# Performance work log

Measured on AMD Instinct MI355X. Metric: run time of the kernel, lower is better.

Reference implementation:

```python
import jax, jax.numpy as jnp
import numpy as np

R, N, B = 3, 8192, 4096
IN_DIM, HID, OUT = 256, 128, 64
EPS = 1e-5


def _bn(x, g, b):
    # BatchNorm1d in training mode: biased batch stats over dim 0
    m = jnp.mean(x, axis=0)
    v = jnp.var(x, axis=0)
    return (x - m) * jax.lax.rsqrt(v + EPS) * g + b


def setup_inputs() -> dict:
    key = jax.random.key(0)
    k1, k2, k3, k4, k5 = jax.random.split(key, 5)
    features = jax.random.normal(k1, (N, IN_DIM), dtype=jnp.float32)
    u = jax.random.uniform(k2, (R, N, N), dtype=jnp.float32)
    adj = (u < 0.01).astype(jnp.float32)
    batch_nodes = jax.random.randint(k3, (B,), 0, N, dtype=jnp.int32)
    w1 = jax.random.uniform(k4, (IN_DIM, HID), dtype=jnp.float32)  # torch.rand init
    w2 = jax.random.uniform(k5, (HID, OUT), dtype=jnp.float32)
    return {
        "features": features, "adj": adj, "batch_nodes": batch_nodes,
        "w1": w1, "w2": w2,
        "gamma1": jnp.ones((IN_DIM,), jnp.float32), "beta1": jnp.zeros((IN_DIM,), jnp.float32),
        "gamma2": jnp.ones((OUT,), jnp.float32), "beta2": jnp.zeros((OUT,), jnp.float32),
    }


def reference(features, adj, batch_nodes, w1, w2, gamma1, beta1, gamma2, beta2):
    # gather batch subgraph
    x = features[batch_nodes]                       # [B, IN_DIM]
    bA = jnp.take(jnp.take(adj, batch_nodes, axis=1), batch_nodes, axis=2)  # [R, B, B]
    xn = _bn(x, gamma1, beta1)                      # shared across relations

    def per_relation(badj):
        A = badj + jnp.eye(B, dtype=badj.dtype)
        # D_mx.inverse().sqrt() of a diagonal degree matrix == diag(deg^-1/2)
        dinv = jax.lax.rsqrt(jnp.sum(A, axis=1))    # [B]
        A_hat = A * dinv[:, None] * dinv[None, :]   # D^-1/2 A D^-1/2
        h1 = jax.nn.sigmoid(jax.nn.elu((A_hat @ xn) @ w1))   # conv1 + sigmoid
        h2 = jax.nn.elu((A_hat @ h1) @ w2)                   # conv2
        return _bn(h2, gamma2, beta2)

    embed = jax.vmap(per_relation)(bA)              # [R, B, OUT]
    return jax.nn.relu(jnp.mean(embed, axis=0))     # [B, OUT]
```

## Files before the change

kernel.cpp:

```cpp
#include <hip/hip_runtime.h>
#include <hip/hip_bf16.h>

#define RR 3
#define NN 8192
#define BB 4096
#define IN_DIM 256
#define HID 128
#define OUT 64
#define CAPD 128
#define EPS 1e-5f
#define MWN (NN / 64)

__global__ __launch_bounds__(1024) void prep_k(const int* __restrict__ bn,
                                               unsigned long long* __restrict__ memb,
                                               unsigned short* __restrict__ rankg,
                                               unsigned short* __restrict__ nodeof,
                                               float* __restrict__ multf,
                                               int* __restrict__ Ucnt,
                                               unsigned short* __restrict__ pos2slot) {
    __shared__ int smult[NN];
    __shared__ unsigned short srank[NN];
    __shared__ unsigned long long smemb[MWN];
    __shared__ int sbase[MWN + 1];
    int t = threadIdx.x;
    for (int u = t; u < NN; u += 1024) smult[u] = 0;
    __syncthreads();
    for (int i = t; i < BB; i += 1024) atomicAdd(&smult[bn[i]], 1);
    __syncthreads();
    if (t < MWN) {
        unsigned long long w = 0;
        for (int b = 0; b < 64; ++b) if (smult[t * 64 + b]) w |= (1ull << b);
        smemb[t] = w;
        memb[t] = w;
    }
    __syncthreads();
    if (t == 0) {
        int acc = 0;
        for (int m = 0; m < MWN; ++m) { sbase[m] = acc; acc += (int)__popcll(smemb[m]); }
        sbase[MWN] = acc;
        *Ucnt = acc;
    }
    __syncthreads();
    if (t < MWN) {
        unsigned long long w = smemb[t];
        int p = sbase[t];
        while (w) {
            int b = __builtin_ctzll(w); w &= w - 1;
            int u = t * 64 + b;
            srank[u] = (unsigned short)p;
            rankg[u] = (unsigned short)p;
            nodeof[p] = (unsigned short)u;
            multf[p]  = (float)smult[u];
            ++p;
        }
    }
    __syncthreads();
    for (int i = t; i < BB; i += 1024) pos2slot[i] = srank[bn[i]];
}

__global__ __launch_bounds__(256) void bn1_stats_k(const float* __restrict__ feat,
                                                   const int* __restrict__ bn,
                                                   float* __restrict__ m1,
                                                   float* __restrict__ rs1) {
    int c = blockIdx.x;
    float s = 0.f, q = 0.f;
    for (int i = threadIdx.x; i < BB; i += 256) {
        float v = feat[(size_t)bn[i] * IN_DIM + c];
        s += v; q += v * v;
    }
    int lane = threadIdx.x & 63, wv = threadIdx.x >> 6;
    for (int o = 32; o; o >>= 1) { s += __shfl_down(s, o); q += __shfl_down(q, o); }
    __shared__ float ps[4], pq[4];
    if (lane == 0) { ps[wv] = s; pq[wv] = q; }
    __syncthreads();
    if (threadIdx.x == 0) {
        float S = ps[0] + ps[1] + ps[2] + ps[3];
        float Q = pq[0] + pq[1] + pq[2] + pq[3];
        float m = S / BB;
        float v = Q / BB - m * m;
        m1[c] = m;
        rs1[c] = rsqrtf(v + EPS);
    }
}

__global__ __launch_bounds__(256) void xn_c_k(const float* __restrict__ feat,
                                              const unsigned short* __restrict__ nodeof,
                                              const int* __restrict__ Ucnt,
                                              const float* __restrict__ m1,
                                              const float* __restrict__ rs1,
                                              const float* __restrict__ g1,
                                              const float* __restrict__ b1,
                                              float* __restrict__ xn_c) {
    int s = blockIdx.x;
    if (s >= *Ucnt) return;
    int u = nodeof[s];
    int c = threadIdx.x;
    float v = feat[(size_t)u * IN_DIM + c];
    xn_c[(size_t)s * IN_DIM + c] = (v - m1[c]) * rs1[c] * g1[c] + b1[c];
}

__global__ __launch_bounds__(256) void build_k(const float* __restrict__ adj,
                                               const unsigned short* __restrict__ nodeof,
                                               const int* __restrict__ Ucnt,
                                               const unsigned long long* __restrict__ memb,
                                               const unsigned short* __restrict__ rankg,
                                               const float* __restrict__ multf,
                                               unsigned short* __restrict__ cols,
                                               int* __restrict__ cnt,
                                               float* __restrict__ dinv) {
    int blk = blockIdx.x;
    int r = blk >> 12, s = blk & (BB - 1);
    if (s >= *Ucnt) return;
    int u = nodeof[s];
    __shared__ unsigned char nib[2048];
    __shared__ unsigned int rawb[256];
    __shared__ unsigned long long sel[MWN];
    __shared__ int sbase[MWN + 1];
    __shared__ float pdeg[4];
    int t = threadIdx.x;
    const float4* ar4 = (const float4*)(adj + ((size_t)r * NN + u) * NN);
    #pragma unroll
    for (int ch = 0; ch < 8; ++ch) {
        float4 v = ar4[ch * 256 + t];
        nib[ch * 256 + t] = (unsigned char)((v.x != 0.f) | ((v.y != 0.f) << 1) |
                                            ((v.z != 0.f) << 2) | ((v.w != 0.f) << 3));
    }
    __syncthreads();
    {
        unsigned long long x = *(const unsigned long long*)&nib[t * 8];
        x = (x | (x >> 4))  & 0x00FF00FF00FF00FFull;
        x = (x | (x >> 8))  & 0x0000FFFF0000FFFFull;
        x = (x | (x >> 16));
        rawb[t] = (unsigned int)x;
    }
    __syncthreads();
    if (t < MWN) {
        unsigned long long w = ((unsigned long long)rawb[2 * t + 1] << 32) | rawb[2 * t];
        sel[t] = w & memb[t];
    }
    __syncthreads();
    if (t < 64) {
        int p0 = (int)__popcll(sel[2 * t]);
        int p1 = (int)__popcll(sel[2 * t + 1]);
        int x = p0 + p1, xs = x;
        for (int o = 1; o < 64; o <<= 1) { int y = __shfl_up(xs, o); if (t >= o) xs += y; }
        sbase[2 * t]     = xs - x;
        sbase[2 * t + 1] = xs - p1;
        if (t == 63) sbase[MWN] = xs;
    }
    __syncthreads();
    float wdeg = 0.f;
    if (t < MWN) {
        unsigned long long w = sel[t];
        int p = sbase[t];
        unsigned short* cb = cols + (size_t)blk * CAPD;
        while (w) {
            int b = __builtin_ctzll(w); w &= w - 1;
            int v = t * 64 + b;
            int rv = rankg[v];
            if (p < CAPD) cb[p] = (unsigned short)rv;
            wdeg += multf[rv];
            ++p;
        }
    }
    int lane = t & 63, wv = t >> 6;
    for (int o = 32; o; o >>= 1) wdeg += __shfl_down(wdeg, o);
    if (lane == 0) pdeg[wv] = wdeg;
    __syncthreads();
    if (t == 0) {
        int tot = sbase[MWN];
        cnt[blk] = tot < CAPD ? tot : CAPD;
        dinv[blk] = rsqrtf(pdeg[0] + pdeg[1] + pdeg[2] + pdeg[3] + 1.0f);
    }
}

__global__ __launch_bounds__(256) void layer1_k(const float* __restrict__ xn_c,
                                                const unsigned short* __restrict__ cols,
                                                const int* __restrict__ cnt,
                                                const float* __restrict__ dinv,
                                                const float* __restrict__ multf,
                                                const int* __restrict__ Ucnt,
                                                const float* __restrict__ w1,
                                                float* __restrict__ h1) {
    int blk = blockIdx.x;
    int r = blk >> 12, s = blk & (BB - 1);
    if (s >= *Ucnt) return;
    int c = threadIdx.x;
    __shared__ unsigned short scl[CAPD];
    __shared__ float swl[CAPD];
    int n = cnt[blk];
    if (c < n) {
        int sl = cols[(size_t)blk * CAPD + c];
        scl[c] = (unsigned short)sl;
        swl[c] = multf[sl] * dinv[(r << 12) + sl];
    }
    __syncthreads();
    float di = dinv[blk];
    float acc = di * xn_c[(size_t)s * IN_DIM + c];
    #pragma unroll 4
    for (int k = 0; k < n; ++k) {
        acc += swl[k] * xn_c[(size_t)scl[k] * IN_DIM + c];
    }
    acc *= di;
    __shared__ float ys[IN_DIM];
    ys[c] = acc;
    __syncthreads();
    if (c < HID) {
        float z = 0.f;
        #pragma unroll 8
        for (int k = 0; k < IN_DIM; ++k) z += ys[k] * w1[k * HID + c];
        float e = z > 0.f ? z : expm1f(z);
        float h = 1.0f / (1.0f + expf(-e));
        h1[(size_t)blk * HID + c] = h;
    }
}

__global__ __launch_bounds__(128) void layer2_k(const float* __restrict__ h1,
                                                const unsigned short* __restrict__ cols,
                                                const int* __restrict__ cnt,
                                                const float* __restrict__ dinv,
                                                const float* __restrict__ multf,
                                                const int* __restrict__ Ucnt,
                                                const float* __restrict__ w2,
                                                float* __restrict__ h2) {
    int blk = blockIdx.x;
    int r = blk >> 12, s = blk & (BB - 1);
    if (s >= *Ucnt) return;
    int c = threadIdx.x;
    __shared__ unsigned short scl[CAPD];
    __shared__ float swl[CAPD];
    int n = cnt[blk];
    if (c < n) {
        int sl = cols[(size_t)blk * CAPD + c];
        scl[c] = (unsigned short)sl;
        swl[c] = multf[sl] * dinv[(r << 12) + sl];
    }
    __syncthreads();
    const float* h1r = h1 + ((size_t)r << 12) * HID;
    float di = dinv[blk];
    float acc = di * h1r[(size_t)s * HID + c];
    #pragma unroll 4
    for (int k = 0; k < n; ++k) {
        acc += swl[k] * h1r[(size_t)scl[k] * HID + c];
    }
    acc *= di;
    __shared__ float ys[HID];
    ys[c] = acc;
    __syncthreads();
    if (c < OUT) {
        float z = 0.f;
        #pragma unroll 8
        for (int k = 0; k < HID; ++k) z += ys[k] * w2[k * OUT + c];
        float e = z > 0.f ? z : expm1f(z);
        h2[(size_t)blk * OUT + c] = e;
    }
}

__global__ __launch_bounds__(256) void bn2_stats_k(const float* __restrict__ h2,
                                                   const float* __restrict__ multf,
                                                   const int* __restrict__ Ucnt,
                                                   float* __restrict__ m2,
                                                   float* __restrict__ rs2) {
    int ro = blockIdx.x;
    int r = ro >> 6, o = ro & (OUT - 1);
    int U = *Ucnt;
    float s = 0.f, q = 0.f;
    for (int sl = threadIdx.x; sl < U; sl += 256) {
        float m = multf[sl];
        float v = h2[(size_t)((r << 12) + sl) * OUT + o];
        s += m * v; q += m * v * v;
    }
    int lane = threadIdx.x & 63, wv = threadIdx.x >> 6;
    for (int off = 32; off; off >>= 1) { s += __shfl_down(s, off); q += __shfl_down(q, off); }
    __shared__ float ps[4], pq[4];
    if (lane == 0) { ps[wv] = s; pq[wv] = q; }
    __syncthreads();
    if (threadIdx.x == 0) {
        float S = ps[0] + ps[1] + ps[2] + ps[3];
        float Q = pq[0] + pq[1] + pq[2] + pq[3];
        float m = S / BB;
        float v = Q / BB - m * m;
        m2[ro] = m;
        rs2[ro] = rsqrtf(v + EPS);
    }
}

__global__ __launch_bounds__(256) void finalize_k(const float* __restrict__ h2,
                                                  const unsigned short* __restrict__ pos2slot,
                                                  const float* __restrict__ m2,
                                                  const float* __restrict__ rs2,
                                                  const float* __restrict__ g2,
                                                  const float* __restrict__ b2,
                                                  float* __restrict__ out) {
    int idx = blockIdx.x * 256 + threadIdx.x;
    if (idx >= BB * OUT) return;
    int i = idx >> 6, o = idx & (OUT - 1);
    int sl = pos2slot[i];
    float s = 0.f;
    for (int r = 0; r < RR; ++r) {
        float v = h2[(size_t)((r << 12) + sl) * OUT + o];
        s += (v - m2[r * OUT + o]) * rs2[r * OUT + o] * g2[o] + b2[o];
    }
    s *= (1.0f / RR);
    out[idx] = s > 0.f ? s : 0.f;
}

extern "C" void kernel_launch(void* const* d_in, const int* in_sizes, int n_in,
                              void* d_out, int out_size, void* d_ws, size_t ws_size,
                              hipStream_t stream) {
    const float* feat = (const float*)d_in[0];
    const float* adj  = (const float*)d_in[1];
    const int*   bn   = (const int*)d_in[2];
    const float* w1   = (const float*)d_in[3];
    const float* w2   = (const float*)d_in[4];
    const float* g1   = (const float*)d_in[5];
    const float* b1   = (const float*)d_in[6];
    const float* g2   = (const float*)d_in[7];
    const float* b2   = (const float*)d_in[8];
    float* out = (float*)d_out;

    char* ws = (char*)d_ws;
    size_t off = 0;
    auto alloc = [&](size_t bytes) { size_t o = off; off += (bytes + 255) & ~(size_t)255; return o; };
    unsigned long long* memb = (unsigned long long*)(ws + alloc(MWN * 8));
    unsigned short* rankg    = (unsigned short*)(ws + alloc(NN * 2));
    unsigned short* nodeof   = (unsigned short*)(ws + alloc(BB * 2));
    float* multf             = (float*)(ws + alloc(BB * 4));
    int* Ucnt                = (int*)(ws + alloc(4));
    unsigned short* pos2slot = (unsigned short*)(ws + alloc(BB * 2));
    float* m1                = (float*)(ws + alloc(IN_DIM * 4));
    float* rs1               = (float*)(ws + alloc(IN_DIM * 4));
    float* m2                = (float*)(ws + alloc(RR * OUT * 4));
    float* rs2               = (float*)(ws + alloc(RR * OUT * 4));
    float* xn_c              = (float*)(ws + alloc((size_t)BB * IN_DIM * 4));
    unsigned short* cols     = (unsigned short*)(ws + alloc((size_t)RR * BB * CAPD * 2));
    int* cnt                 = (int*)(ws + alloc((size_t)RR * BB * 4));
    float* dinv              = (float*)(ws + alloc((size_t)RR * BB * 4));
    float* h1                = (float*)(ws + alloc((size_t)RR * BB * HID * 4));
    float* h2                = (float*)(ws + alloc((size_t)RR * BB * OUT * 4));

    prep_k<<<1, 1024, 0, stream>>>(bn, memb, rankg, nodeof, multf, Ucnt, pos2slot);
    bn1_stats_k<<<IN_DIM, 256, 0, stream>>>(feat, bn, m1, rs1);
    xn_c_k<<<BB, 256, 0, stream>>>(feat, nodeof, Ucnt, m1, rs1, g1, b1, xn_c);
    build_k<<<RR * BB, 256, 0, stream>>>(adj, nodeof, Ucnt, memb, rankg, multf, cols, cnt, dinv);
    layer1_k<<<RR * BB, 256, 0, stream>>>(xn_c, cols, cnt, dinv, multf, Ucnt, w1, h1);
    layer2_k<<<RR * BB, 128, 0, stream>>>(h1, cols, cnt, dinv, multf, Ucnt, w2, h2);
    bn2_stats_k<<<RR * OUT, 256, 0, stream>>>(h2, multf, Ucnt, m2, rs2);
    finalize_k<<<(BB * OUT + 255) / 256, 256, 0, stream>>>(h2, pos2slot, m2, rs2, g2, b2, out);
}
```

Baseline: 176.5 us.

## Process four nodes per block in GCN layers and split BN1 stats reduction

layer1 and layer2 now handle four compacted nodes per block, one wavefront per node, using float4/float2 vectorized neighbor gathers. Each W1/W2 weight load is shared across two or four node rows, and block count and launch overhead drop. BN1 statistics are now computed over unique nodes weighted by multiplicity, using a two-stage partial and final reduction instead of one block per column with strided gathers. This adds an extra kernel launch and leaves a longer serial loop per wavefront when a node has high degree.

```diff
diff --git a/kernel.cpp b/kernel.cpp
--- a/kernel.cpp
+++ b/kernel.cpp
@@ -58,29 +58,38 @@
     for (int i = t; i < BB; i += 1024) pos2slot[i] = srank[bn[i]];
 }
 
-__global__ __launch_bounds__(256) void bn1_stats_k(const float* __restrict__ feat,
-                                                   const int* __restrict__ bn,
+__global__ __launch_bounds__(256) void bn1_partial_k(const float* __restrict__ feat,
+                                                     const unsigned short* __restrict__ nodeof,
+                                                     const float* __restrict__ multf,
+                                                     const int* __restrict__ Ucnt,
+                                                     float* __restrict__ partial) {
+    int b = blockIdx.x;
+    int c = threadIdx.x;
+    int U = *Ucnt;
+    float s = 0.f, q = 0.f;
+    for (int t = 0; t < 64; ++t) {
+        int sl = b * 64 + t;
+        if (sl >= U) break;
+        float m = multf[sl];
+        float v = feat[(size_t)nodeof[sl] * IN_DIM + c];
+        s += m * v; q += m * v * v;
+    }
+    partial[(size_t)(2 * b) * IN_DIM + c]     = s;
+    partial[(size_t)(2 * b + 1) * IN_DIM + c] = q;
+}
+
+__global__ __launch_bounds__(256) void bn1_final_k(const float* __restrict__ partial,
                                                    float* __restrict__ m1,
                                                    float* __restrict__ rs1) {
-    int c = blockIdx.x;
-    float s = 0.f, q = 0.f;
-    for (int i = threadIdx.x; i < BB; i += 256) {
-        float v = feat[(size_t)bn[i] * IN_DIM + c];
-        s += v; q += v * v;
-    }
-    int lane = threadIdx.x & 63, wv = threadIdx.x >> 6;
-    for (int o = 32; o; o >>= 1) { s += __shfl_down(s, o); q += __shfl_down(q, o); }
-    __shared__ float ps[4], pq[4];
-    if (lane == 0) { ps[wv] = s; pq[wv] = q; }
-    __syncthreads();
-    if (threadIdx.x == 0) {
-        float S = ps[0] + ps[1] + ps[2] + ps[3];
-        float Q = pq[0] + pq[1] + pq[2] + pq[3];
-        float m = S / BB;
-        float v = Q / BB - m * m;
-        m1[c] = m;
-        rs1[c] = rsqrtf(v + EPS);
-    }
+    int c = threadIdx.x;
+    float S = 0.f, Q = 0.f;
+    for (int b = 0; b < 64; ++b) {
+        S += partial[(size_t)(2 * b) * IN_DIM + c];
+        Q += partial[(size_t)(2 * b + 1) * IN_DIM + c];
+    }
+    float m = S / BB;
+    m1[c] = m;
+    rs1[c] = rsqrtf(Q / BB - m * m + EPS);
 }
 
 __global__ __launch_bounds__(256) void xn_c_k(const float* __restrict__ feat,
@@ -183,39 +192,55 @@
                                                 const float* __restrict__ w1,
                                                 float* __restrict__ h1) {
     int blk = blockIdx.x;
-    int r = blk >> 12, s = blk & (BB - 1);
-    if (s >= *Ucnt) return;
-    int c = threadIdx.x;
-    __shared__ unsigned short scl[CAPD];
-    __shared__ float swl[CAPD];
-    int n = cnt[blk];
-    if (c < n) {
-        int sl = cols[(size_t)blk * CAPD + c];
-        scl[c] = (unsigned short)sl;
-        swl[c] = multf[sl] * dinv[(r << 12) + sl];
-    }
-    __syncthreads();
-    float di = dinv[blk];
-    float acc = di * xn_c[(size_t)s * IN_DIM + c];
-    #pragma unroll 4
-    for (int k = 0; k < n; ++k) {
-        acc += swl[k] * xn_c[(size_t)scl[k] * IN_DIM + c];
-    }
-    acc *= di;
-    __shared__ float ys[IN_DIM];
-    ys[c] = acc;
-    __syncthreads();
-    if (c < HID) {
-        float z = 0.f;
-        #pragma unroll 8
-        for (int k = 0; k < IN_DIM; ++k) z += ys[k] * w1[k * HID + c];
-        float e = z > 0.f ? z : expm1f(z);
-        float h = 1.0f / (1.0f + expf(-e));
-        h1[(size_t)blk * HID + c] = h;
-    }
-}
-
-__global__ __launch_bounds__(128) void layer2_k(const float* __restrict__ h1,
+    int r = blk >> 10, base = (blk & 1023) << 2;
+    int U = *Ucnt;
+    int tid = threadIdx.x, lane = tid & 63, wv = tid >> 6;
+    __shared__ unsigned short scl[4][CAPD];
+    __shared__ float swl[4][CAPD];
+    __shared__ float ys[4][IN_DIM];
+    __shared__ float sdi[4];
+    int slot = base + wv;
+    int n = (slot < U) ? cnt[(r << 12) + slot] : 0;
+    if (lane == 0) sdi[wv] = (slot < U) ? dinv[(r << 12) + slot] : 0.f;
+    size_t cb = ((size_t)(r << 12) + slot) * CAPD;
+    for (int idx = lane; idx < n; idx += 64) {
+        int sl = cols[cb + idx];
+        scl[wv][idx] = (unsigned short)sl;
+        swl[wv][idx] = multf[sl] * dinv[(r << 12) + sl];
+    }
+    __syncthreads();
+    {
+        float di = sdi[wv];
+        float4 acc = make_float4(0.f, 0.f, 0.f, 0.f);
+        if (slot < U) {
+            float4 xv = ((const float4*)(xn_c + (size_t)slot * IN_DIM))[lane];
+            acc.x = di * xv.x; acc.y = di * xv.y; acc.z = di * xv.z; acc.w = di * xv.w;
+        }
+        #pragma unroll 4
+        for (int k = 0; k < n; ++k) {
+            float4 xv = ((const float4*)(xn_c + (size_t)scl[wv][k] * IN_DIM))[lane];
+            float wk = swl[wv][k];
+            acc.x += wk * xv.x; acc.y += wk * xv.y; acc.z += wk * xv.z; acc.w += wk * xv.w;
+        }
+        acc.x *= di; acc.y *= di; acc.z *= di; acc.w *= di;
+        *(float4*)&ys[wv][lane * 4] = acc;
+    }
+    __syncthreads();
+    int c = tid & 127, h = tid >> 7;
+    float z0 = 0.f, z1 = 0.f;
+    #pragma unroll 8
+    for (int k = 0; k < IN_DIM; ++k) {
+        float wvl = w1[k * HID + c];
+        z0 += ys[h][k] * wvl;
+        z1 += ys[h + 2][k] * wvl;
+    }
+    float e0 = z0 > 0.f ? z0 : expm1f(z0);
+    h1[((size_t)(r << 12) + base + h) * HID + c] = 1.f / (1.f + expf(-e0));
+    float e1 = z1 > 0.f ? z1 : expm1f(z1);
+    h1[((size_t)(r << 12) + base + h + 2) * HID + c] = 1.f / (1.f + expf(-e1));
+}
+
+__global__ __launch_bounds__(256) void layer2_k(const float* __restrict__ h1,
                                                 const unsigned short* __restrict__ cols,
                                                 const int* __restrict__ cnt,
                                                 const float* __restrict__ dinv,
@@ -224,36 +249,47 @@
                                                 const float* __restrict__ w2,
                                                 float* __restrict__ h2) {
     int blk = blockIdx.x;
-    int r = blk >> 12, s = blk & (BB - 1);
-    if (s >= *Ucnt) return;
-    int c = threadIdx.x;
-    __shared__ unsigned short scl[CAPD];
-    __shared__ float swl[CAPD];
-    int n = cnt[blk];
-    if (c < n) {
-        int sl = cols[(size_t)blk * CAPD + c];
-        scl[c] = (unsigned short)sl;
-        swl[c] = multf[sl] * dinv[(r << 12) + sl];
-    }
-    __syncthreads();
-    const float* h1r = h1 + ((size_t)r << 12) * HID;
-    float di = dinv[blk];
-    float acc = di * h1r[(size_t)s * HID + c];
-    #pragma unroll 4
-    for (int k = 0; k < n; ++k) {
-        acc += swl[k] * h1r[(size_t)scl[k] * HID + c];
-    }
-    acc *= di;
-    __shared__ float ys[HID];
-    ys[c] = acc;
-    __syncthreads();
-    if (c < OUT) {
-        float z = 0.f;
-        #pragma unroll 8
-        for (int k = 0; k < HID; ++k) z += ys[k] * w2[k * OUT + c];
-        float e = z > 0.f ? z : expm1f(z);
-        h2[(size_t)blk * OUT + c] = e;
-    }
+    int r = blk >> 10, base = (blk & 1023) << 2;
+    int U = *Ucnt;
+    int tid = threadIdx.x, lane = tid & 63, wv = tid >> 6;
+    __shared__ unsigned short scl[4][CAPD];
+    __shared__ float swl[4][CAPD];
+    __shared__ float ys[4][HID];
+    __shared__ float sdi[4];
+    int slot = base + wv;
+    int n = (slot < U) ? cnt[(r << 12) + slot] : 0;
+    if (lane == 0) sdi[wv] = (slot < U) ? dinv[(r << 12) + slot] : 0.f;
+    size_t cb = ((size_t)(r << 12) + slot) * CAPD;
+    for (int idx = lane; idx < n; idx += 64) {
+        int sl = cols[cb + idx];
+        scl[wv][idx] = (unsigned short)sl;
+        swl[wv][idx] = multf[sl] * dinv[(r << 12) + sl];
+    }
+    __syncthreads();
+    const float* h1r = h1 + ((size_t)(r << 12)) * HID;
+    {
+        float di = sdi[wv];
+        float2 acc = make_float2(0.f, 0.f);
+        if (slot < U) {
+            float2 xv = ((const float2*)(h1r + (size_t)slot * HID))[lane];
+            acc.x = di * xv.x; acc.y = di * xv.y;
+        }
+        #pragma unroll 4
+        for (int k = 0; k < n; ++k) {
+            float2 xv = ((const float2*)(h1r + (size_t)scl[wv][k] * HID))[lane];
+            float wk = swl[wv][k];
+            acc.x += wk * xv.x; acc.y += wk * xv.y;
+        }
+        acc.x *= di; acc.y *= di;
+        ys[wv][lane * 2] = acc.x; ys[wv][lane * 2 + 1] = acc.y;
+    }
+    __syncthreads();
+    int c = tid & 63, g = tid >> 6;
+    float z = 0.f;
+    #pragma unroll 8
+    for (int k = 0; k < HID; ++k) z += ys[g][k] * w2[k * OUT + c];
+    float e = z > 0.f ? z : expm1f(z);
+    h2[((size_t)(r << 12) + base + g) * OUT + c] = e;
 }
 
 __global__ __launch_bounds__(256) void bn2_stats_k(const float* __restrict__ h2,
@@ -328,6 +364,7 @@
     float* multf             = (float*)(ws + alloc(BB * 4));
     int* Ucnt                = (int*)(ws + alloc(4));
     unsigned short* pos2slot = (unsigned short*)(ws + alloc(BB * 2));
+    float* partial           = (float*)(ws + alloc(128 * IN_DIM * 4));
     float* m1                = (float*)(ws + alloc(IN_DIM * 4));
     float* rs1               = (float*)(ws + alloc(IN_DIM * 4));
     float* m2                = (float*)(ws + alloc(RR * OUT * 4));
@@ -340,11 +377,12 @@
     float* h2                = (float*)(ws + alloc((size_t)RR * BB * OUT * 4));
 
     prep_k<<<1, 1024, 0, stream>>>(bn, memb, rankg, nodeof, multf, Ucnt, pos2slot);
-    bn1_stats_k<<<IN_DIM, 256, 0, stream>>>(feat, bn, m1, rs1);
+    bn1_partial_k<<<64, 256, 0, stream>>>(feat, nodeof, multf, Ucnt, partial);
+    bn1_final_k<<<1, 256, 0, stream>>>(partial, m1, rs1);
     xn_c_k<<<BB, 256, 0, stream>>>(feat, nodeof, Ucnt, m1, rs1, g1, b1, xn_c);
     build_k<<<RR * BB, 256, 0, stream>>>(adj, nodeof, Ucnt, memb, rankg, multf, cols, cnt, dinv);
-    layer1_k<<<RR * BB, 256, 0, stream>>>(xn_c, cols, cnt, dinv, multf, Ucnt, w1, h1);
-    layer2_k<<<RR * BB, 128, 0, stream>>>(h1, cols, cnt, dinv, multf, Ucnt, w2, h2);
+    layer1_k<<<RR * (BB / 4), 256, 0, stream>>>(xn_c, cols, cnt, dinv, multf, Ucnt, w1, h1);
+    layer2_k<<<RR * (BB / 4), 256, 0, stream>>>(h1, cols, cnt, dinv, multf, Ucnt, w2, h2);
     bn2_stats_k<<<RR * OUT, 256, 0, stream>>>(h2, multf, Ucnt, m2, rs2);
     finalize_k<<<(BB * OUT + 255) / 256, 256, 0, stream>>>(h2, pos2slot, m2, rs2, g2, b2, out);
 }
```

New measurement: 198.5 us. 12.5% more time.

## Split aggregation and dense projection into separate kernels with batched row tiles

Applied to the files above, without the earlier changes.

The fused per-row layer kernels, which ran the sparse aggregation and the weight matvec in the same block, are split in two. The aggregation kernels now write the aggregated features to new intermediate buffers. New MLP kernels then multiply tiles of 16 rows by w1 and w2, so each weight load is reused across 8 or 4 rows per thread. Previously each row re-read the whole weight matrix with only half or a quarter of its threads active. The cost is two extra launches and extra global traffic to write and re-read the intermediates.

```diff
diff --git a/kernel.cpp b/kernel.cpp
--- a/kernel.cpp
+++ b/kernel.cpp
@@ -10,6 +10,7 @@
 #define CAPD 128
 #define EPS 1e-5f
 #define MWN (NN / 64)
+#define MLPB 16
 
 __global__ __launch_bounds__(1024) void prep_k(const int* __restrict__ bn,
                                                unsigned long long* __restrict__ memb,
@@ -174,14 +175,13 @@
     }
 }
 
-__global__ __launch_bounds__(256) void layer1_k(const float* __restrict__ xn_c,
-                                                const unsigned short* __restrict__ cols,
-                                                const int* __restrict__ cnt,
-                                                const float* __restrict__ dinv,
-                                                const float* __restrict__ multf,
-                                                const int* __restrict__ Ucnt,
-                                                const float* __restrict__ w1,
-                                                float* __restrict__ h1) {
+__global__ __launch_bounds__(256) void layer1_agg_k(const float* __restrict__ xn_c,
+                                                    const unsigned short* __restrict__ cols,
+                                                    const int* __restrict__ cnt,
+                                                    const float* __restrict__ dinv,
+                                                    const float* __restrict__ multf,
+                                                    const int* __restrict__ Ucnt,
+                                                    float* __restrict__ y1) {
     int blk = blockIdx.x;
     int r = blk >> 12, s = blk & (BB - 1);
     if (s >= *Ucnt) return;
@@ -201,28 +201,50 @@
     for (int k = 0; k < n; ++k) {
         acc += swl[k] * xn_c[(size_t)scl[k] * IN_DIM + c];
     }
-    acc *= di;
-    __shared__ float ys[IN_DIM];
-    ys[c] = acc;
-    __syncthreads();
-    if (c < HID) {
-        float z = 0.f;
-        #pragma unroll 8
-        for (int k = 0; k < IN_DIM; ++k) z += ys[k] * w1[k * HID + c];
-        float e = z > 0.f ? z : expm1f(z);
-        float h = 1.0f / (1.0f + expf(-e));
-        h1[(size_t)blk * HID + c] = h;
-    }
-}
-
-__global__ __launch_bounds__(128) void layer2_k(const float* __restrict__ h1,
-                                                const unsigned short* __restrict__ cols,
-                                                const int* __restrict__ cnt,
-                                                const float* __restrict__ dinv,
-                                                const float* __restrict__ multf,
-                                                const int* __restrict__ Ucnt,
-                                                const float* __restrict__ w2,
-                                                float* __restrict__ h2) {
+    y1[(size_t)blk * IN_DIM + c] = acc * di;
+}
+
+__global__ __launch_bounds__(256) void mlp1_k(const float* __restrict__ y1,
+                                              const int* __restrict__ Ucnt,
+                                              const float* __restrict__ w1,
+                                              float* __restrict__ h1) {
+    int blk = blockIdx.x;
+    int r = blk / (BB / MLPB), base = (blk % (BB / MLPB)) * MLPB;
+    int U = *Ucnt;
+    if (base >= U) return;
+    int t = threadIdx.x;
+    __shared__ float ys[MLPB][IN_DIM];
+    #pragma unroll
+    for (int s = 0; s < MLPB; ++s) {
+        int slot = base + s;
+        ys[s][t] = (slot < U) ? y1[((size_t)(r << 12) + slot) * IN_DIM + t] : 0.f;
+    }
+    __syncthreads();
+    int c = t & 127, g = t >> 7;
+    float acc[8] = {0.f};
+    for (int k = 0; k < IN_DIM; ++k) {
+        float wv = w1[k * HID + c];
+        #pragma unroll
+        for (int j = 0; j < 8; ++j) acc[j] += ys[g * 8 + j][k] * wv;
+    }
+    #pragma unroll
+    for (int j = 0; j < 8; ++j) {
+        int slot = base + g * 8 + j;
+        if (slot < U) {
+            float z = acc[j];
+            float e = z > 0.f ? z : expm1f(z);
+            h1[((size_t)(r << 12) + slot) * HID + c] = 1.f / (1.f + expf(-e));
+        }
+    }
+}
+
+__global__ __launch_bounds__(128) void layer2_agg_k(const float* __restrict__ h1,
+                                                    const unsigned short* __restrict__ cols,
+                                                    const int* __restrict__ cnt,
+                                                    const float* __restrict__ dinv,
+                                                    const float* __restrict__ multf,
+                                                    const int* __restrict__ Ucnt,
+                                                    float* __restrict__ y2) {
     int blk = blockIdx.x;
     int r = blk >> 12, s = blk & (BB - 1);
     if (s >= *Ucnt) return;
@@ -236,23 +258,46 @@
         swl[c] = multf[sl] * dinv[(r << 12) + sl];
     }
     __syncthreads();
-    const float* h1r = h1 + ((size_t)r << 12) * HID;
+    const float* h1r = h1 + ((size_t)(r << 12)) * HID;
     float di = dinv[blk];
     float acc = di * h1r[(size_t)s * HID + c];
     #pragma unroll 4
     for (int k = 0; k < n; ++k) {
         acc += swl[k] * h1r[(size_t)scl[k] * HID + c];
     }
-    acc *= di;
-    __shared__ float ys[HID];
-    ys[c] = acc;
-    __syncthreads();
-    if (c < OUT) {
-        float z = 0.f;
-        #pragma unroll 8
-        for (int k = 0; k < HID; ++k) z += ys[k] * w2[k * OUT + c];
-        float e = z > 0.f ? z : expm1f(z);
-        h2[(size_t)blk * OUT + c] = e;
+    y2[(size_t)blk * HID + c] = acc * di;
+}
+
+__global__ __launch_bounds__(256) void mlp2_k(const float* __restrict__ y2,
+                                              const int* __restrict__ Ucnt,
+                                              const float* __restrict__ w2,
+                                              float* __restrict__ h2) {
+    int blk = blockIdx.x;
+    int r = blk / (BB / MLPB), base = (blk % (BB / MLPB)) * MLPB;
+    int U = *Ucnt;
+    if (base >= U) return;
+    int t = threadIdx.x;
+    __shared__ float ys[MLPB][HID];
+    #pragma unroll
+    for (int s = t >> 7; s < MLPB; s += 2) {
+        int slot = base + s;
+        ys[s][t & 127] = (slot < U) ? y2[((size_t)(r << 12) + slot) * HID + (t & 127)] : 0.f;
+    }
+    __syncthreads();
+    int c = t & 63, g = t >> 6;
+    float acc[4] = {0.f};
+    for (int k = 0; k < HID; ++k) {
+        float wv = w2[k * OUT + c];
+        #pragma unroll
+        for (int j = 0; j < 4; ++j) acc[j] += ys[g * 4 + j][k] * wv;
+    }
+    #pragma unroll
+    for (int j = 0; j < 4; ++j) {
+        int slot = base + g * 4 + j;
+        if (slot < U) {
+            float z = acc[j];
+            h2[((size_t)(r << 12) + slot) * OUT + c] = z > 0.f ? z : expm1f(z);
+        }
     }
 }
 
@@ -336,15 +381,19 @@
     unsigned short* cols     = (unsigned short*)(ws + alloc((size_t)RR * BB * CAPD * 2));
     int* cnt                 = (int*)(ws + alloc((size_t)RR * BB * 4));
     float* dinv              = (float*)(ws + alloc((size_t)RR * BB * 4));
+    float* y1                = (float*)(ws + alloc((size_t)RR * BB * IN_DIM * 4));
     float* h1                = (float*)(ws + alloc((size_t)RR * BB * HID * 4));
+    float* y2                = (float*)(ws + alloc((size_t)RR * BB * HID * 4));
     float* h2                = (float*)(ws + alloc((size_t)RR * BB * OUT * 4));
 
     prep_k<<<1, 1024, 0, stream>>>(bn, memb, rankg, nodeof, multf, Ucnt, pos2slot);
     bn1_stats_k<<<IN_DIM, 256, 0, stream>>>(feat, bn, m1, rs1);
     xn_c_k<<<BB, 256, 0, stream>>>(feat, nodeof, Ucnt, m1, rs1, g1, b1, xn_c);
     build_k<<<RR * BB, 256, 0, stream>>>(adj, nodeof, Ucnt, memb, rankg, multf, cols, cnt, dinv);
-    layer1_k<<<RR * BB, 256, 0, stream>>>(xn_c, cols, cnt, dinv, multf, Ucnt, w1, h1);
-    layer2_k<<<RR * BB, 128, 0, stream>>>(h1, cols, cnt, dinv, multf, Ucnt, w2, h2);
+    layer1_agg_k<<<RR * BB, 256, 0, stream>>>(xn_c, cols, cnt, dinv, multf, Ucnt, y1);
+    mlp1_k<<<RR * (BB / MLPB), 256, 0, stream>>>(y1, Ucnt, w1, h1);
+    layer2_agg_k<<<RR * BB, 128, 0, stream>>>(h1, cols, cnt, dinv, multf, Ucnt, y2);
+    mlp2_k<<<RR * (BB / MLPB), 256, 0, stream>>>(y2, Ucnt, w2, h2);
     bn2_stats_k<<<RR * OUT, 256, 0, stream>>>(h2, multf, Ucnt, m2, rs2);
     finalize_k<<<(BB * OUT + 255) / 256, 256, 0, stream>>>(h2, pos2slot, m2, rs2, g2, b2, out);
 }
```

Result: faster. 172.1 us (-2.5%).
